# Kernel optimization log

Hardware: AMD Instinct MI355X
Metric: run time of the kernel (lower is better)

## Reference

```python
import jax, jax.numpy as jnp
import numpy as np

D_MODEL = 256
D_STATE = 64
D_CONV = 4
EXPAND = 2
HEADDIM = 16
D_INNER = EXPAND * D_MODEL            # 512
NHEADS = D_INNER // HEADDIM           # 32
CONV_DIM = D_INNER + 2 * D_STATE      # 640 (ngroups=1)
D_IN_PROJ = 2 * D_INNER + 2 * D_STATE + NHEADS  # 1184
BATCH = 256
SEQ = 200


def _ln(x, g, b, eps=1e-12):
    m = jnp.mean(x, axis=-1, keepdims=True)
    v = jnp.mean((x - m) ** 2, axis=-1, keepdims=True)
    return (x - m) * jax.lax.rsqrt(v + eps) * g + b


def setup_inputs() -> dict:
    key = jax.random.key(0)
    ks = jax.random.split(key, 16)
    def gn(i, shape, s=0.02):
        return jax.random.normal(ks[i], shape, jnp.float32) * s
    return {
        "input_tensor": jax.random.normal(ks[0], (BATCH, SEQ, D_MODEL), jnp.float32),
        # Mamba2 params
        "in_proj_w": gn(1, (D_MODEL, D_IN_PROJ)),
        "conv_w": gn(2, (CONV_DIM, D_CONV), 0.1),
        "conv_b": jnp.zeros((CONV_DIM,), jnp.float32),
        "dt_bias": gn(3, (NHEADS,), 0.1),
        "A_log": jnp.log(jax.random.uniform(ks[4], (NHEADS,), jnp.float32, 1.0, 16.0)),
        "D_skip": jnp.ones((NHEADS,), jnp.float32),
        "rms_w": jnp.ones((D_INNER,), jnp.float32),
        "out_proj_w": gn(5, (D_INNER, D_MODEL)),
        # Layer norms / mixers
        "ln_g": jnp.ones((D_MODEL,), jnp.float32),
        "ln_b": jnp.zeros((D_MODEL,), jnp.float32),
        "filt_w": gn(6, (1, SEQ // 2 + 1, D_MODEL, 2), 0.02),
        "filt_ln_g": jnp.ones((D_MODEL,), jnp.float32),
        "filt_ln_b": jnp.zeros((D_MODEL,), jnp.float32),
        "alpha": jax.random.uniform(ks[7], (D_MODEL,), jnp.float32),
        "beta": jax.random.uniform(ks[8], (D_MODEL,), jnp.float32),
        # FFN
        "ffn_w1": gn(9, (D_MODEL, 4 * D_MODEL)),
        "ffn_b1": jnp.zeros((4 * D_MODEL,), jnp.float32),
        "ffn_w2": gn(10, (4 * D_MODEL, D_MODEL)),
        "ffn_b2": jnp.zeros((D_MODEL,), jnp.float32),
        "ffn_ln_g": jnp.ones((D_MODEL,), jnp.float32),
        "ffn_ln_b": jnp.zeros((D_MODEL,), jnp.float32),
    }


def _mamba2(x, in_proj_w, conv_w, conv_b, dt_bias, A_log, D_skip, rms_w, out_proj_w):
    b, l, _ = x.shape
    zxbcdt = x @ in_proj_w                                  # [b,l,1184]
    z, xBC, dt = jnp.split(zxbcdt, [D_INNER, D_INNER + CONV_DIM], axis=-1)
    # depthwise causal conv over time + SiLU
    xp = jnp.pad(xBC, ((0, 0), (D_CONV - 1, 0), (0, 0)))
    conv = conv_b + sum(conv_w[:, k] * xp[:, k:k + l, :] for k in range(D_CONV))
    xBC = jax.nn.silu(conv)
    xs, Bm, Cm = jnp.split(xBC, [D_INNER, D_INNER + D_STATE], axis=-1)
    xh = xs.reshape(b, l, NHEADS, HEADDIM)
    dt = jax.nn.softplus(dt + dt_bias)                      # [b,l,h]
    A = -jnp.exp(A_log)                                     # [h]
    dA = jnp.exp(dt * A)                                    # [b,l,h]
    dtx = dt[..., None] * xh                                # [b,l,h,p]

    def step(state, inp):
        dA_t, dtx_t, B_t, C_t = inp
        # state: [b,h,p,n]
        state = dA_t[:, :, None, None] * state + dtx_t[..., None] * B_t[:, None, None, :]
        y_t = jnp.einsum('bhpn,bn->bhp', state, C_t)
        return state, y_t

    state0 = jnp.zeros((b, NHEADS, HEADDIM, D_STATE), x.dtype)
    _, y = jax.lax.scan(step, state0,
                        (jnp.moveaxis(dA, 1, 0), jnp.moveaxis(dtx, 1, 0),
                         jnp.moveaxis(Bm, 1, 0), jnp.moveaxis(Cm, 1, 0)))
    y = jnp.moveaxis(y, 0, 1) + D_skip[None, None, :, None] * xh   # skip connection
    y = y.reshape(b, l, D_INNER)
    # gated RMSNorm: rmsnorm(y * silu(z)) * w
    g = y * jax.nn.silu(z)
    g = g * jax.lax.rsqrt(jnp.mean(g * g, axis=-1, keepdims=True) + 1e-5) * rms_w
    return g @ out_proj_w


def reference(input_tensor, in_proj_w, conv_w, conv_b, dt_bias, A_log, D_skip,
              rms_w, out_proj_w, ln_g, ln_b, filt_w, filt_ln_g, filt_ln_b,
              alpha, beta, ffn_w1, ffn_b1, ffn_w2, ffn_b2, ffn_ln_g, ffn_ln_b):
    x = input_tensor
    h1 = _mamba2(x, in_proj_w, conv_w, conv_b, dt_bias, A_log, D_skip, rms_w, out_proj_w)
    h1 = _ln(h1 + x, ln_g, ln_b)
    # FFT filter branch
    xf = jnp.fft.rfft(x, axis=1, norm='ortho')
    w = filt_w[..., 0] + 1j * filt_w[..., 1]                # [1,101,d]
    xi = jnp.fft.irfft(xf * w, n=SEQ, axis=1, norm='ortho').astype(x.dtype)
    h2 = _ln(xi + x, filt_ln_g, filt_ln_b)
    h = alpha * h1 + beta * h2
    hid = jax.nn.gelu(h @ ffn_w1 + ffn_b1, approximate=False) @ ffn_w2 + ffn_b2
    return _ln(hid + h, ffn_ln_g, ffn_ln_b)
```

## Files before the change

### kernel.cpp

```cpp
#include <hip/hip_runtime.h>
#include <math.h>

#define BATCHN 256
#define SEQ 200
#define DMODEL 256
#define DINNER 512
#define NH 32
#define HD 16
#define DSTATE 64
#define DINPROJ 1184
#define XBCLD 672
#define BL (BATCHN*SEQ)
#define NF 101
#define XBASE 655360
#define TC 20
#define NCH 10
#define XIOFF 8500000

typedef __attribute__((ext_vector_type(8))) short bf16x8;
typedef __attribute__((ext_vector_type(4))) float f32x4;

__device__ inline unsigned short f2bf(float f) {
    union { float f; unsigned u; } v; v.f = f;
    unsigned r = v.u + 0x7FFFu + ((v.u >> 16) & 1u);
    return (unsigned short)(r >> 16);
}
__device__ inline float bf2f(unsigned short h) {
    union { unsigned u; float f; } v; v.u = ((unsigned)h) << 16;
    return v.f;
}

#define GLOAD16(src, dst) __builtin_amdgcn_global_load_lds( \
    (const __attribute__((address_space(1))) void*)(src),   \
    (__attribute__((address_space(3))) void*)(dst), 16, 0, 0)

__global__ void init_dft_kernel(unsigned short* __restrict__ EF, unsigned short* __restrict__ EI)
{
    const float ang = 6.28318530717958647692f / 200.0f;
    int idx = blockIdx.x * 256 + threadIdx.x;
    if (idx < 256 * SEQ) {
        int f = idx / SEQ, t = idx - f * SEQ;
        float v;
        if (f <= 100) { int ph = (f * t) % 200; v = cosf(ang * (float)ph); }
        else if (f <= 201) { int ff = f - 101; int ph = (ff * t) % 200; v = -sinf(ang * (float)ph); }
        else v = 0.f;
        EF[idx] = f2bf(v);
    } else if (idx < 256 * SEQ + 256 * 256) {
        int j2 = idx - 256 * SEQ;
        int t = j2 >> 8, j = j2 & 255;
        float v;
        if (t >= 200) v = 0.f;
        else if (j == 0) v = 1.0f / 200.0f;
        else if (j == 100) v = ((t & 1) ? -1.0f : 1.0f) / 200.0f;
        else if (j < 100) { int ph = (j * t) % 200; v = 2.0f * cosf(ang * (float)ph) / 200.0f; }
        else if (j >= 202 || j == 101 || j == 201) v = 0.0f;
        else { int f = j - 101; int ph = (f * t) % 200; v = -2.0f * sinf(ang * (float)ph) / 200.0f; }
        EI[j2] = f2bf(v);
    }
}

#define S0 303104
#define S1 131072
#define S2 262144
#define S3 262144
#define S4 1638400
__global__ void setup_kernel(const float* __restrict__ ipw, const float* __restrict__ opw,
                             const float* __restrict__ w1, const float* __restrict__ w2,
                             const float* __restrict__ X,
                             unsigned short* __restrict__ wTall, unsigned short* __restrict__ opwT,
                             unsigned short* __restrict__ w1T, unsigned short* __restrict__ w2T,
                             unsigned short* __restrict__ xbf)
{
    long long idx = (long long)blockIdx.x * 256 + threadIdx.x;
    if (idx < S0) { int n = (int)(idx / 256), k = (int)(idx % 256);
        wTall[idx] = f2bf(ipw[(long long)k * DINPROJ + n]); return; }
    idx -= S0;
    if (idx < S1) { int n = (int)(idx / 512), k = (int)(idx % 512);
        opwT[idx] = f2bf(opw[(long long)k * 256 + n]); return; }
    idx -= S1;
    if (idx < S2) { int n = (int)(idx / 256), k = (int)(idx % 256);
        w1T[idx] = f2bf(w1[(long long)k * 1024 + n]); return; }
    idx -= S2;
    if (idx < S3) { int n = (int)(idx / 1024), k = (int)(idx % 1024);
        w2T[idx] = f2bf(w2[(long long)k * 256 + n]); return; }
    idx -= S3;
    if (idx < S4) {
        long long i = idx * 8;
        float4 a = ((const float4*)(X + i))[0];
        float4 b = ((const float4*)(X + i))[1];
        uint4 o;
        o.x = (unsigned)f2bf(a.x) | ((unsigned)f2bf(a.y) << 16);
        o.y = (unsigned)f2bf(a.z) | ((unsigned)f2bf(a.w) << 16);
        o.z = (unsigned)f2bf(b.x) | ((unsigned)f2bf(b.y) << 16);
        o.w = (unsigned)f2bf(b.z) | ((unsigned)f2bf(b.w) << 16);
        *(uint4*)(xbf + i) = o;
    }
}

__global__ void xT_kernel(const float* __restrict__ X, unsigned short* __restrict__ XT)
{
    __shared__ float tile[32][33];
    int b = blockIdx.z, t0 = blockIdx.x * 32, d0 = blockIdx.y * 32;
    int tx = threadIdx.x & 31, ty = threadIdx.x >> 5;
    const float* xb = X + (long long)b * SEQ * DMODEL;
#pragma unroll
    for (int i = 0; i < 4; i++) {
        int t = t0 + ty + i * 8;
        tile[ty + i * 8][tx] = (t < SEQ) ? xb[(long long)t * DMODEL + d0 + tx] : 0.f;
    }
    __syncthreads();
    unsigned short* xtb = XT + (long long)b * DMODEL * SEQ;
#pragma unroll
    for (int i = 0; i < 4; i++) {
        int d = d0 + ty + i * 8;
        int t = t0 + tx;
        if (t < SEQ) xtb[(long long)d * SEQ + t] = f2bf(tile[tx][ty + i * 8]);
    }
}

template<int ACT, int CBF>
__global__ __launch_bounds__(256) void mgemm_kernel(
    const unsigned short* __restrict__ Ab, const unsigned short* __restrict__ BTp,
    void* __restrict__ Cp, const float* __restrict__ bias,
    int M, int N, int K, int lda, int ldbt, int ldc,
    long long sA, long long sBT, long long sC)
{
    __shared__ unsigned short As[128 * 32];
    __shared__ unsigned short Bs[128 * 32];
    const unsigned short* Aa = Ab + (long long)blockIdx.z * sA;
    const unsigned short* Bt = BTp + (long long)blockIdx.z * sBT;
    float* Cf = (float*)Cp + (CBF ? 0 : (long long)blockIdx.z * sC);
    unsigned short* Cb = (unsigned short*)Cp + (CBF ? (long long)blockIdx.z * sC : 0);

    int m0 = blockIdx.y * 128, n0 = blockIdx.x * 128;
    int tid = threadIdx.x;
    int srow = tid >> 1, skb = (tid & 1) * 16;
    int w = tid >> 6, l = tid & 63;
    int wr = w >> 1, wc = w & 1;
    int fr = l & 15, fk = l >> 4;
    int glr = (w << 4) + (l >> 2);
    int glc = (l & 3) << 3;
    bool fullM = (m0 + 128 <= M);
    bool fullN = (n0 + 128 <= N);

    f32x4 acc[4][4] = {};

    for (int k0 = 0; k0 < K; k0 += 32) {
        bool kedge = (k0 + 32 > K);
        if (fullM && !kedge) {
            GLOAD16(Aa + (long long)(m0 + glr) * lda + k0 + glc,      &As[w << 9]);
            GLOAD16(Aa + (long long)(m0 + 64 + glr) * lda + k0 + glc, &As[2048 + (w << 9)]);
        } else {
            int gm = m0 + srow;
            unsigned short* dst = &As[srow * 32 + skb];
#pragma unroll
            for (int i = 0; i < 16; i++) {
                int gk = k0 + skb + i;
                dst[i] = (gm < M && gk < K) ? Aa[(long long)gm * lda + gk] : (unsigned short)0;
            }
        }
        if (fullN && !kedge) {
            GLOAD16(Bt + (long long)(n0 + glr) * ldbt + k0 + glc,      &Bs[w << 9]);
            GLOAD16(Bt + (long long)(n0 + 64 + glr) * ldbt + k0 + glc, &Bs[2048 + (w << 9)]);
        } else {
            int gn = n0 + srow;
            unsigned short* dst = &Bs[srow * 32 + skb];
#pragma unroll
            for (int i = 0; i < 16; i++) {
                int gk = k0 + skb + i;
                dst[i] = (gn < N && gk < K) ? Bt[(long long)gn * ldbt + gk] : (unsigned short)0;
            }
        }
        __syncthreads();
        bf16x8 a[4], b[4];
#pragma unroll
        for (int i = 0; i < 4; i++) {
            a[i] = *(const bf16x8*)&As[(wr * 64 + i * 16 + fr) * 32 + fk * 8];
            b[i] = *(const bf16x8*)&Bs[(wc * 64 + i * 16 + fr) * 32 + fk * 8];
        }
#pragma unroll
        for (int i = 0; i < 4; i++)
#pragma unroll
            for (int j = 0; j < 4; j++)
                acc[i][j] = __builtin_amdgcn_mfma_f32_16x16x32_bf16(a[i], b[j], acc[i][j], 0, 0, 0);
        __syncthreads();
    }

#pragma unroll
    for (int i = 0; i < 4; i++) {
        int gr0 = m0 + wr * 64 + i * 16 + fk * 4;
#pragma unroll
        for (int j = 0; j < 4; j++) {
            int gc = n0 + wc * 64 + j * 16 + fr;
            if (gc >= N) continue;
            float bv = bias ? bias[gc] : 0.f;
#pragma unroll
            for (int r = 0; r < 4; r++) {
                int gr = gr0 + r;
                if (gr >= M) continue;
                float v = acc[i][j][r] + bv;
                if (ACT == 1) v = 0.5f * v * (1.f + erff(v * 0.70710678118654752f));
                long long ci = (long long)gr * ldc + gc;
                if (CBF) Cb[ci] = f2bf(v);
                else Cf[ci] = v;
            }
        }
    }
}

__global__ __launch_bounds__(256) void mgemm_proj(
    const unsigned short* __restrict__ Aa, const unsigned short* __restrict__ Bt,
    float* __restrict__ XBCout, unsigned short* __restrict__ Zout)
{
    __shared__ unsigned short As[128 * 32];
    __shared__ unsigned short Bs[128 * 32];
    const int N = DINPROJ;
    int m0 = blockIdx.y * 128, n0 = blockIdx.x * 128;
    int tid = threadIdx.x;
    int srow = tid >> 1, skb = (tid & 1) * 16;
    int w = tid >> 6, l = tid & 63;
    int wr = w >> 1, wc = w & 1;
    int fr = l & 15, fk = l >> 4;
    int glr = (w << 4) + (l >> 2);
    int glc = (l & 3) << 3;
    bool fullN = (n0 + 128 <= N);

    f32x4 acc[4][4] = {};

    for (int k0 = 0; k0 < 256; k0 += 32) {
        GLOAD16(Aa + (long long)(m0 + glr) * 256 + k0 + glc,      &As[w << 9]);
        GLOAD16(Aa + (long long)(m0 + 64 + glr) * 256 + k0 + glc, &As[2048 + (w << 9)]);
        if (fullN) {
            GLOAD16(Bt + (long long)(n0 + glr) * 256 + k0 + glc,      &Bs[w << 9]);
            GLOAD16(Bt + (long long)(n0 + 64 + glr) * 256 + k0 + glc, &Bs[2048 + (w << 9)]);
        } else {
            int gn = n0 + srow;
            unsigned short* dst = &Bs[srow * 32 + skb];
#pragma unroll
            for (int i = 0; i < 16; i++)
                dst[i] = (gn < N) ? Bt[(long long)gn * 256 + k0 + skb + i] : (unsigned short)0;
        }
        __syncthreads();
        bf16x8 a[4], b[4];
#pragma unroll
        for (int i = 0; i < 4; i++) {
            a[i] = *(const bf16x8*)&As[(wr * 64 + i * 16 + fr) * 32 + fk * 8];
            b[i] = *(const bf16x8*)&Bs[(wc * 64 + i * 16 + fr) * 32 + fk * 8];
        }
#pragma unroll
        for (int i = 0; i < 4; i++)
#pragma unroll
            for (int j = 0; j < 4; j++)
                acc[i][j] = __builtin_amdgcn_mfma_f32_16x16x32_bf16(a[i], b[j], acc[i][j], 0, 0, 0);
        __syncthreads();
    }

#pragma unroll
    for (int i = 0; i < 4; i++) {
        int gr0 = m0 + wr * 64 + i * 16 + fk * 4;
#pragma unroll
        for (int j = 0; j < 4; j++) {
            int gc = n0 + wc * 64 + j * 16 + fr;
            if (gc >= N) continue;
#pragma unroll
            for (int r = 0; r < 4; r++) {
                int gr = gr0 + r;
                float v = acc[i][j][r];
                if (gc < 512) Zout[(long long)gr * 512 + gc] = f2bf(v);
                else XBCout[(long long)gr * XBCLD + (gc - 512)] = v;
            }
        }
    }
}

__global__ __launch_bounds__(256) void convbc2_kernel(
    const float* __restrict__ XBC, const float* __restrict__ conv_w,
    const float* __restrict__ conv_b, const float* __restrict__ dt_bias,
    const float* __restrict__ A_log,
    float* __restrict__ BCb, float* __restrict__ DTb, float* __restrict__ DAb,
    float* __restrict__ BCF)
{
    __shared__ float swin[28][128];
    __shared__ float sv[25][128];
    int tid = threadIdx.x;
    int bid = blockIdx.x;
    int b = bid >> 3, c = bid & 7;
    int t0 = c * 25;
    long long rowb = (long long)b * SEQ;
    for (int i = tid; i < 28 * 32; i += 256) {
        int r = i >> 5, q = i & 31;
        int t = t0 - 3 + r;
        float4 v = (t >= 0) ? ((const float4*)(XBC + (rowb + t) * XBCLD + 512))[q]
                            : (float4){0.f, 0.f, 0.f, 0.f};
        ((float4*)&swin[r][0])[q] = v;
    }
    for (int i = tid; i < 25 * 32; i += 256) {
        int r = i >> 5, h = i & 31;
        long long row = rowb + t0 + r;
        float draw = XBC[row * XBCLD + 640 + h] + dt_bias[h];
        float dtv = (draw > 20.f) ? draw : log1pf(__expf(draw));
        DTb[row * NH + h] = dtv;
        DAb[row * NH + h] = __expf(-__expf(A_log[h]) * dtv);
    }
    __syncthreads();
    for (int i = tid; i < 25 * 128; i += 256) {
        int r = i >> 7, ch = i & 127;
        int gch = 512 + ch;
        float acc = conv_b[gch];
#pragma unroll
        for (int k = 0; k < 4; k++)
            acc = fmaf(conv_w[gch * 4 + k], swin[r + k][ch], acc);
        float v = acc * __builtin_amdgcn_rcpf(1.f + __expf(-acc));
        BCb[(rowb + t0 + r) * 128 + ch] = v;
        sv[r][ch] = v;
    }
    __syncthreads();
    int wv = tid >> 6, lane = tid & 63;
    for (int r = wv; r < 25; r += 4) {
        float prod = sv[r][lane] * sv[r][64 + lane];
#pragma unroll
        for (int m = 1; m < 64; m <<= 1) prod += __shfl_xor(prod, m);
        if (lane == 0) BCF[rowb + t0 + r] = prod;
    }
}

__device__ __forceinline__ void sstep2(
    float raw, float dtv, float da, float bc,
    const float4& qb0, const float4& qb1, const float4& qb2, const float4& qb3,
    const float4& qc0, const float4& qc1, const float4& qc2, const float4& qc3,
    float cw0, float cw1, float cw2, float cw3, float cb, float ds,
    float* st, float& w0, float& w1, float& w2,
    int lane, float* __restrict__ yaddr)
{
    float cvv = cb + cw0 * w0 + cw1 * w1 + cw2 * w2 + cw3 * raw;
    float xhv = cvv * __builtin_amdgcn_rcpf(1.f + __expf(-cvv));
    w0 = w1; w1 = w2; w2 = raw;
    float xv = dtv * xhv;
    float p0 = st[0]  * qc0.x;
    float p1 = st[1]  * qc0.y;
    float p2 = st[2]  * qc0.z;
    float p3 = st[3]  * qc0.w;
    p0 = fmaf(st[4],  qc1.x, p0);
    p1 = fmaf(st[5],  qc1.y, p1);
    p2 = fmaf(st[6],  qc1.z, p2);
    p3 = fmaf(st[7],  qc1.w, p3);
    p0 = fmaf(st[8],  qc2.x, p0);
    p1 = fmaf(st[9],  qc2.y, p1);
    p2 = fmaf(st[10], qc2.z, p2);
    p3 = fmaf(st[11], qc2.w, p3);
    p0 = fmaf(st[12], qc3.x, p0);
    p1 = fmaf(st[13], qc3.y, p1);
    p2 = fmaf(st[14], qc3.z, p2);
    p3 = fmaf(st[15], qc3.w, p3);
    st[0]  = fmaf(da, st[0],  xv * qb0.x);
    st[1]  = fmaf(da, st[1],  xv * qb0.y);
    st[2]  = fmaf(da, st[2],  xv * qb0.z);
    st[3]  = fmaf(da, st[3],  xv * qb0.w);
    st[4]  = fmaf(da, st[4],  xv * qb1.x);
    st[5]  = fmaf(da, st[5],  xv * qb1.y);
    st[6]  = fmaf(da, st[6],  xv * qb1.z);
    st[7]  = fmaf(da, st[7],  xv * qb1.w);
    st[8]  = fmaf(da, st[8],  xv * qb2.x);
    st[9]  = fmaf(da, st[9],  xv * qb2.y);
    st[10] = fmaf(da, st[10], xv * qb2.z);
    st[11] = fmaf(da, st[11], xv * qb2.w);
    st[12] = fmaf(da, st[12], xv * qb3.x);
    st[13] = fmaf(da, st[13], xv * qb3.y);
    st[14] = fmaf(da, st[14], xv * qb3.z);
    st[15] = fmaf(da, st[15], xv * qb3.w);
    float part = (p0 + p1) + (p2 + p3);
    part += __shfl_xor(part, 16);
    part += __shfl_xor(part, 32);
    if (lane < HD) *yaddr = fmaf(da, part, fmaf(xv, bc, ds * xhv));
}

__global__ __launch_bounds__(256) void scan7b_kernel(
    const float* __restrict__ DTb, const float* __restrict__ DAb,
    float* __restrict__ XBC, const float* __restrict__ BCb,
    const float* __restrict__ Dsk,
    const float* __restrict__ conv_w, const float* __restrict__ conv_b,
    const float* __restrict__ BCF)
{
    __shared__ float sbc[2][TC][128];
    __shared__ unsigned short sx[2][TC][128];
    __shared__ float sdt[2][TC][8];
    __shared__ float sda[2][TC][8];
    __shared__ float sbcf[2][TC];
    int tid = threadIdx.x;
    int wv = tid >> 6, lane = tid & 63;
    int bid = blockIdx.x;
    int b = bid >> 2, hq = (bid & 3) * 8;
    long long rowb = (long long)b * SEQ;

    for (int i = tid; i < TC * 32; i += 256) {
        int r = i >> 5, c = i & 31;
        ((float4*)&sbc[0][r][0])[c] = ((const float4*)(BCb + (rowb + r) * 128))[c];
    }
    for (int i = tid; i < TC * 64; i += 256) {
        int r = i >> 6, c2 = i & 63;
        float2 v = *(const float2*)(XBC + (rowb + r) * XBCLD + hq * 16 + (c2 << 1));
        *(unsigned*)&sx[0][r][c2 << 1] = (unsigned)f2bf(v.x) | ((unsigned)f2bf(v.y) << 16);
    }
    for (int i = tid; i < TC * 8; i += 256) {
        int t = i >> 3, j = i & 7;
        sdt[0][t][j] = DTb[(rowb + t) * NH + hq + j];
        sda[0][t][j] = DAb[(rowb + t) * NH + hq + j];
    }
    if (tid < TC) sbcf[0][tid] = BCF[rowb + tid];
    __syncthreads();

    int p = lane & 15, g = lane >> 4;
    int hA = hq + wv, hB = hq + 4 + wv;
    int chA = hA * HD + p, chB = hB * HD + p;
    float cwA0 = conv_w[chA * 4 + 0], cwA1 = conv_w[chA * 4 + 1];
    float cwA2 = conv_w[chA * 4 + 2], cwA3 = conv_w[chA * 4 + 3];
    float cbA = conv_b[chA];
    float cwB0 = conv_w[chB * 4 + 0], cwB1 = conv_w[chB * 4 + 1];
    float cwB2 = conv_w[chB * 4 + 2], cwB3 = conv_w[chB * 4 + 3];
    float cbB = conv_b[chB];
    float dsA = Dsk[hA], dsB = Dsk[hB];
    int xcA = wv * 16 + p, xcB = (4 + wv) * 16 + p;
    float* ypA = XBC + rowb * XBCLD + hA * HD + p;
    float* ypB = XBC + rowb * XBCLD + hB * HD + p;
    float stA[16], stB[16];
#pragma unroll
    for (int r = 0; r < 16; r++) { stA[r] = 0.f; stB[r] = 0.f; }
    float wA0 = 0.f, wA1 = 0.f, wA2 = 0.f;
    float wB0 = 0.f, wB1 = 0.f, wB2 = 0.f;

    for (int c = 0; c < NCH; c++) {
        int cur = c & 1;
        if (c + 1 < NCH) {
            int nb = cur ^ 1;
            long long tb = rowb + (c + 1) * TC;
            for (int i = tid; i < TC * 32; i += 256) {
                int r = i >> 5, cc = i & 31;
                ((float4*)&sbc[nb][r][0])[cc] = ((const float4*)(BCb + (tb + r) * 128))[cc];
            }
            for (int i = tid; i < TC * 64; i += 256) {
                int r = i >> 6, c2 = i & 63;
                float2 v = *(const float2*)(XBC + (tb + r) * XBCLD + hq * 16 + (c2 << 1));
                *(unsigned*)&sx[nb][r][c2 << 1] = (unsigned)f2bf(v.x) | ((unsigned)f2bf(v.y) << 16);
            }
            for (int i = tid; i < TC * 8; i += 256) {
                int t = i >> 3, j = i & 7;
                sdt[nb][t][j] = DTb[(tb + t) * NH + hq + j];
                sda[nb][t][j] = DAb[(tb + t) * NH + hq + j];
            }
            if (tid < TC) sbcf[nb][tid] = BCF[tb + tid];
        }
        int tbase = c * TC;
        for (int t = 0; t < TC; t++) {
            int gt = tbase + t;
            const float4* qb = (const float4*)&sbc[cur][t][g * 16];
            const float4* qc = (const float4*)&sbc[cur][t][64 + g * 16];
            float4 qb0 = qb[0], qb1 = qb[1], qb2 = qb[2], qb3 = qb[3];
            float4 qc0 = qc[0], qc1 = qc[1], qc2 = qc[2], qc3 = qc[3];
            float rawA = bf2f(sx[cur][t][xcA]);
            float rawB = bf2f(sx[cur][t][xcB]);
            float bc = sbcf[cur][t];
            sstep2(rawA, sdt[cur][t][wv], sda[cur][t][wv], bc,
                   qb0, qb1, qb2, qb3, qc0, qc1, qc2, qc3,
                   cwA0, cwA1, cwA2, cwA3, cbA, dsA, stA, wA0, wA1, wA2,
                   lane, ypA + (long long)gt * XBCLD);
            sstep2(rawB, sdt[cur][t][4 + wv], sda[cur][t][4 + wv], bc,
                   qb0, qb1, qb2, qb3, qc0, qc1, qc2, qc3,
                   cwB0, cwB1, cwB2, cwB3, cbB, dsB, stB, wB0, wB1, wB2,
                   lane, ypB + (long long)gt * XBCLD);
        }
        __syncthreads();
    }
}

__global__ __launch_bounds__(256) void gate_kernel(
    float* __restrict__ XBC, const unsigned short* __restrict__ Zbf,
    const float* __restrict__ rms_w)
{
    int row = blockIdx.x * 4 + (threadIdx.x >> 6);
    int lane = threadIdx.x & 63;
    float* yrow = XBC + (long long)row * XBCLD + lane * 8;
    const unsigned short* zrow = Zbf + (long long)row * 512 + lane * 8;
    float4 y0 = ((const float4*)yrow)[0];
    float4 y1 = ((const float4*)yrow)[1];
    uint4 zq = ((const uint4*)zrow)[0];
    float yv[8] = { y0.x, y0.y, y0.z, y0.w, y1.x, y1.y, y1.z, y1.w };
    float zv[8];
    zv[0] = bf2f((unsigned short)(zq.x & 0xFFFF)); zv[1] = bf2f((unsigned short)(zq.x >> 16));
    zv[2] = bf2f((unsigned short)(zq.y & 0xFFFF)); zv[3] = bf2f((unsigned short)(zq.y >> 16));
    zv[4] = bf2f((unsigned short)(zq.z & 0xFFFF)); zv[5] = bf2f((unsigned short)(zq.z >> 16));
    zv[6] = bf2f((unsigned short)(zq.w & 0xFFFF)); zv[7] = bf2f((unsigned short)(zq.w >> 16));
    float a[8]; float ss = 0.f;
#pragma unroll
    for (int i = 0; i < 8; i++) {
        float z = zv[i];
        a[i] = yv[i] * (z * __builtin_amdgcn_rcpf(1.f + __expf(-z)));
        ss = fmaf(a[i], a[i], ss);
    }
#pragma unroll
    for (int m = 1; m < 64; m <<= 1) ss += __shfl_xor(ss, m);
    float sc = rsqrtf(ss * (1.f / 512.f) + 1e-5f);
    const float* rw = rms_w + lane * 8;
    float4 r0 = ((const float4*)rw)[0];
    float4 r1 = ((const float4*)rw)[1];
    float rv[8] = { r0.x, r0.y, r0.z, r0.w, r1.x, r1.y, r1.z, r1.w };
    uint4 o;
    o.x = (unsigned)f2bf(a[0] * sc * rv[0]) | ((unsigned)f2bf(a[1] * sc * rv[1]) << 16);
    o.y = (unsigned)f2bf(a[2] * sc * rv[2]) | ((unsigned)f2bf(a[3] * sc * rv[3]) << 16);
    o.z = (unsigned)f2bf(a[4] * sc * rv[4]) | ((unsigned)f2bf(a[5] * sc * rv[5]) << 16);
    o.w = (unsigned)f2bf(a[6] * sc * rv[6]) | ((unsigned)f2bf(a[7] * sc * rv[7]) << 16);
    unsigned short* grow = (unsigned short*)(XBC + (long long)row * XBCLD);
    ((uint4*)grow)[lane] = o;
}

__global__ void lnadd_bb_kernel(const unsigned short* __restrict__ A, const unsigned short* __restrict__ Bb,
                                const float* __restrict__ g, const float* __restrict__ be,
                                float* __restrict__ O)
{
    int row = blockIdx.x * 4 + (threadIdx.x >> 6);
    int lane = threadIdx.x & 63;
    long long base = (long long)row * DMODEL + lane * 4;
    float v[4]; float s1 = 0.f;
#pragma unroll
    for (int i = 0; i < 4; i++) { float a = bf2f(A[base + i]) + bf2f(Bb[base + i]); v[i] = a; s1 += a; }
#pragma unroll
    for (int m = 1; m < 64; m <<= 1) s1 += __shfl_xor(s1, m);
    float mean = s1 * (1.f / 256.f);
    float s2 = 0.f;
#pragma unroll
    for (int i = 0; i < 4; i++) { float d = v[i] - mean; s2 = fmaf(d, d, s2); }
#pragma unroll
    for (int m = 1; m < 64; m <<= 1) s2 += __shfl_xor(s2, m);
    float r = rsqrtf(s2 * (1.f / 256.f) + 1e-12f);
#pragma unroll
    for (int i = 0; i < 4; i++)
        O[base + i] = (v[i] - mean) * r * g[lane * 4 + i] + be[lane * 4 + i];
}

__global__ void combine2_kernel(const float* __restrict__ XI, const float* __restrict__ X,
                                const float* __restrict__ MO, unsigned short* __restrict__ HB,
                                const float* __restrict__ lg, const float* __restrict__ lb,
                                const float* __restrict__ fg, const float* __restrict__ fb,
                                const float* __restrict__ al, const float* __restrict__ bt)
{
    int row = blockIdx.x * 4 + (threadIdx.x >> 6);
    int lane = threadIdx.x & 63;
    long long base = (long long)row * DMODEL + lane * 4;
    int bb = row / SEQ, ll = row - bb * SEQ;
    long long xib = (long long)bb * 65536 + ll * 256 + lane * 4;
    float u[4], v[4]; float su = 0.f, sv = 0.f;
#pragma unroll
    for (int i = 0; i < 4; i++) {
        float xv = X[base + i];
        float a = MO[base + i] + xv;
        float b = XI[xib + i] + xv;
        u[i] = a; v[i] = b; su += a; sv += b;
    }
#pragma unroll
    for (int m = 1; m < 64; m <<= 1) { su += __shfl_xor(su, m); sv += __shfl_xor(sv, m); }
    float mu = su * (1.f / 256.f), mv = sv * (1.f / 256.f);
    float qu = 0.f, qv = 0.f;
#pragma unroll
    for (int i = 0; i < 4; i++) {
        float du = u[i] - mu; qu = fmaf(du, du, qu);
        float dv = v[i] - mv; qv = fmaf(dv, dv, qv);
    }
#pragma unroll
    for (int m = 1; m < 64; m <<= 1) { qu += __shfl_xor(qu, m); qv += __shfl_xor(qv, m); }
    float ru = rsqrtf(qu * (1.f / 256.f) + 1e-12f);
    float rv = rsqrtf(qv * (1.f / 256.f) + 1e-12f);
#pragma unroll
    for (int i = 0; i < 4; i++) {
        int d = lane * 4 + i;
        float h1 = (u[i] - mu) * ru * lg[d] + lb[d];
        float h2 = (v[i] - mv) * rv * fg[d] + fb[d];
        float h = al[d] * h1 + bt[d] * h2;
        HB[base + i] = f2bf(h);
    }
}

__global__ void filt_kernel(unsigned short* __restrict__ XF, const float* __restrict__ W)
{
    long long idx = (long long)blockIdx.x * 256 + threadIdx.x;
    if (idx >= (long long)BATCHN * DMODEL * NF) return;
    int f = (int)(idx % NF);
    int d = (int)((idx / NF) % DMODEL);
    int b = (int)(idx / ((long long)NF * DMODEL));
    long long base = ((long long)b * DMODEL + d) * 256;
    float re = bf2f(XF[base + f]);
    float im = bf2f(XF[base + 101 + f]);
    float wr = W[((long long)f * DMODEL + d) * 2];
    float wi = W[((long long)f * DMODEL + d) * 2 + 1];
    XF[base + f]       = f2bf(re * wr - im * wi);
    XF[base + 101 + f] = f2bf(re * wi + im * wr);
}

extern "C" void kernel_launch(void* const* d_in, const int* in_sizes, int n_in,
                              void* d_out, int out_size, void* d_ws, size_t ws_size,
                              hipStream_t stream)
{
    const float* x          = (const float*)d_in[0];
    const float* in_proj_w  = (const float*)d_in[1];
    const float* conv_w     = (const float*)d_in[2];
    const float* conv_b     = (const float*)d_in[3];
    const float* dt_bias    = (const float*)d_in[4];
    const float* A_log      = (const float*)d_in[5];
    const float* D_skip     = (const float*)d_in[6];
    const float* rms_w      = (const float*)d_in[7];
    const float* out_proj_w = (const float*)d_in[8];
    const float* ln_g       = (const float*)d_in[9];
    const float* ln_b       = (const float*)d_in[10];
    const float* filt_w     = (const float*)d_in[11];
    const float* filt_ln_g  = (const float*)d_in[12];
    const float* filt_ln_b  = (const float*)d_in[13];
    const float* alpha      = (const float*)d_in[14];
    const float* beta       = (const float*)d_in[15];
    const float* ffn_w1     = (const float*)d_in[16];
    const float* ffn_b1     = (const float*)d_in[17];
    const float* ffn_w2     = (const float*)d_in[18];
    const float* ffn_b2     = (const float*)d_in[19];
    const float* ffn_ln_g   = (const float*)d_in[20];
    const float* ffn_ln_b   = (const float*)d_in[21];
    float* out = (float*)d_out;
    float* ws = (float*)d_ws;

    unsigned short* WP    = (unsigned short*)(ws + 81920);
    unsigned short* wTall = WP;
    unsigned short* opwT  = wTall + 1184 * 256;
    unsigned short* w1T   = opwT + 256 * 512;
    unsigned short* w2T   = w1T + 1024 * 256;
    unsigned short* EFbf  = w2T + 256 * 1024;
    unsigned short* EIbf  = EFbf + 256 * SEQ;
    float* XBC = ws + XBASE;
    float* BCb = XBC + (long long)BL * XBCLD;
    float* DTb = BCb + (long long)BL * 128;
    float* DAb = DTb + (long long)BL * NH;
    float* MO  = DAb + (long long)BL * NH;
    float* BCF = MO + (long long)BL * DMODEL;
    unsigned short* Zbf = (unsigned short*)MO;
    unsigned short* xbf  = (unsigned short*)BCb;
    unsigned short* xTbf = (unsigned short*)BCb;
    unsigned short* MObf = (unsigned short*)BCb;
    unsigned short* Gbf = (unsigned short*)XBC;
    unsigned short* XFT = (unsigned short*)XBC;
    float* XI  = XBC + XIOFF;
    unsigned short* HID = (unsigned short*)XBC;
    unsigned short* FFO = (unsigned short*)(XBC + 26500000);

    init_dft_kernel<<<dim3((256 * SEQ + 256 * 256 + 255) / 256), dim3(256), 0, stream>>>(EFbf, EIbf);
    setup_kernel<<<dim3((S0 + S1 + S2 + S3 + S4) / 256), dim3(256), 0, stream>>>(
        in_proj_w, out_proj_w, ffn_w1, ffn_w2, x, wTall, opwT, w1T, w2T, xbf);

    mgemm_proj<<<dim3(10, BL / 128), dim3(256), 0, stream>>>(xbf, wTall, XBC, Zbf);

    convbc2_kernel<<<dim3(BATCHN * 8), dim3(256), 0, stream>>>(XBC, conv_w, conv_b, dt_bias,
                                                               A_log, BCb, DTb, DAb, BCF);

    scan7b_kernel<<<dim3(BATCHN * 4), dim3(256), 0, stream>>>(DTb, DAb, XBC, BCb, D_skip,
                                                              conv_w, conv_b, BCF);

    xT_kernel<<<dim3(7, 8, BATCHN), dim3(256), 0, stream>>>(x, xTbf);

    gate_kernel<<<dim3(BL / 4), dim3(256), 0, stream>>>(XBC, Zbf, rms_w);

    mgemm_kernel<0,0><<<dim3(2, BL / 128, 1), dim3(256), 0, stream>>>(
        Gbf, opwT, MO, nullptr, BL, 256, 512, 1344, 512, 256, 0, 0, 0);

    mgemm_kernel<0,1><<<dim3(2, 2, BATCHN), dim3(256), 0, stream>>>(
        xTbf, EFbf, XFT, nullptr, 256, 256, SEQ, SEQ, SEQ, 256,
        (long long)DMODEL * SEQ, 0, 65536);

    filt_kernel<<<dim3((BATCHN * DMODEL * NF + 255) / 256), dim3(256), 0, stream>>>(XFT, filt_w);

    mgemm_kernel<0,0><<<dim3(2, 2, BATCHN), dim3(256), 0, stream>>>(
        EIbf, XFT, XI, nullptr, 256, 256, 256, 256, 256, 256,
        0, 65536, 65536);

    combine2_kernel<<<dim3(BL / 4), dim3(256), 0, stream>>>(XI, x, MO, MObf,
                                                            ln_g, ln_b, filt_ln_g, filt_ln_b,
                                                            alpha, beta);

    mgemm_kernel<1,1><<<dim3(8, BL / 128, 1), dim3(256), 0, stream>>>(
        MObf, w1T, HID, ffn_b1, BL, 1024, 256, 256, 256, 1024, 0, 0, 0);

    mgemm_kernel<0,1><<<dim3(2, BL / 128, 1), dim3(256), 0, stream>>>(
        HID, w2T, FFO, ffn_b2, BL, 256, 1024, 1024, 1024, 256, 0, 0, 0);

    lnadd_bb_kernel<<<dim3(BL / 4), dim3(256), 0, stream>>>(FFO, MObf, ffn_ln_g, ffn_ln_b, out);
}
```

Before: 790.5 us.

## Double GEMM K-tile to 64 and store inverse-DFT output as bf16

```diff
diff --git a/kernel.cpp b/kernel.cpp
--- a/kernel.cpp
+++ b/kernel.cpp
@@ -125,8 +125,8 @@
     int M, int N, int K, int lda, int ldbt, int ldc,
     long long sA, long long sBT, long long sC)
 {
-    __shared__ unsigned short As[128 * 32];
-    __shared__ unsigned short Bs[128 * 32];
+    __shared__ unsigned short As[128 * 64];
+    __shared__ unsigned short Bs[128 * 64];
     const unsigned short* Aa = Ab + (long long)blockIdx.z * sA;
     const unsigned short* Bt = BTp + (long long)blockIdx.z * sBT;
     float* Cf = (float*)Cp + (CBF ? 0 : (long long)blockIdx.z * sC);
@@ -134,55 +134,62 @@
 
     int m0 = blockIdx.y * 128, n0 = blockIdx.x * 128;
     int tid = threadIdx.x;
-    int srow = tid >> 1, skb = (tid & 1) * 16;
     int w = tid >> 6, l = tid & 63;
     int wr = w >> 1, wc = w & 1;
     int fr = l & 15, fk = l >> 4;
-    int glr = (w << 4) + (l >> 2);
-    int glc = (l & 3) << 3;
+    int grow = (w & 1) * 64 + (l >> 2);
+    int gcol = (w >> 1) * 32 + (l & 3) * 8;
+    int srow = tid >> 1, shalf = tid & 1;
     bool fullM = (m0 + 128 <= M);
     bool fullN = (n0 + 128 <= N);
 
     f32x4 acc[4][4] = {};
 
-    for (int k0 = 0; k0 < K; k0 += 32) {
-        bool kedge = (k0 + 32 > K);
+    for (int k0 = 0; k0 < K; k0 += 64) {
+        bool kedge = (k0 + 64 > K);
         if (fullM && !kedge) {
-            GLOAD16(Aa + (long long)(m0 + glr) * lda + k0 + glc,      &As[w << 9]);
-            GLOAD16(Aa + (long long)(m0 + 64 + glr) * lda + k0 + glc, &As[2048 + (w << 9)]);
+#pragma unroll
+            for (int q = 0; q < 4; q++)
+                GLOAD16(Aa + (long long)(m0 + grow + q * 16) * lda + k0 + gcol,
+                        &As[w * 2048 + q * 512]);
         } else {
             int gm = m0 + srow;
-            unsigned short* dst = &As[srow * 32 + skb];
-#pragma unroll
-            for (int i = 0; i < 16; i++) {
-                int gk = k0 + skb + i;
+            unsigned short* dst = &As[shalf * 4096 + srow * 32];
+#pragma unroll
+            for (int i = 0; i < 32; i++) {
+                int gk = k0 + shalf * 32 + i;
                 dst[i] = (gm < M && gk < K) ? Aa[(long long)gm * lda + gk] : (unsigned short)0;
             }
         }
         if (fullN && !kedge) {
-            GLOAD16(Bt + (long long)(n0 + glr) * ldbt + k0 + glc,      &Bs[w << 9]);
-            GLOAD16(Bt + (long long)(n0 + 64 + glr) * ldbt + k0 + glc, &Bs[2048 + (w << 9)]);
+#pragma unroll
+            for (int q = 0; q < 4; q++)
+                GLOAD16(Bt + (long long)(n0 + grow + q * 16) * ldbt + k0 + gcol,
+                        &Bs[w * 2048 + q * 512]);
         } else {
             int gn = n0 + srow;
-            unsigned short* dst = &Bs[srow * 32 + skb];
-#pragma unroll
-            for (int i = 0; i < 16; i++) {
-                int gk = k0 + skb + i;
+            unsigned short* dst = &Bs[shalf * 4096 + srow * 32];
+#pragma unroll
+            for (int i = 0; i < 32; i++) {
+                int gk = k0 + shalf * 32 + i;
                 dst[i] = (gn < N && gk < K) ? Bt[(long long)gn * ldbt + gk] : (unsigned short)0;
             }
         }
         __syncthreads();
-        bf16x8 a[4], b[4];
-#pragma unroll
-        for (int i = 0; i < 4; i++) {
-            a[i] = *(const bf16x8*)&As[(wr * 64 + i * 16 + fr) * 32 + fk * 8];
-            b[i] = *(const bf16x8*)&Bs[(wc * 64 + i * 16 + fr) * 32 + fk * 8];
-        }
-#pragma unroll
-        for (int i = 0; i < 4; i++)
-#pragma unroll
-            for (int j = 0; j < 4; j++)
-                acc[i][j] = __builtin_amdgcn_mfma_f32_16x16x32_bf16(a[i], b[j], acc[i][j], 0, 0, 0);
+#pragma unroll
+        for (int s = 0; s < 2; s++) {
+            bf16x8 a[4], b[4];
+#pragma unroll
+            for (int i = 0; i < 4; i++) {
+                a[i] = *(const bf16x8*)&As[s * 4096 + (wr * 64 + i * 16 + fr) * 32 + fk * 8];
+                b[i] = *(const bf16x8*)&Bs[s * 4096 + (wc * 64 + i * 16 + fr) * 32 + fk * 8];
+            }
+#pragma unroll
+            for (int i = 0; i < 4; i++)
+#pragma unroll
+                for (int j = 0; j < 4; j++)
+                    acc[i][j] = __builtin_amdgcn_mfma_f32_16x16x32_bf16(a[i], b[j], acc[i][j], 0, 0, 0);
+        }
         __syncthreads();
     }
 
@@ -212,46 +219,55 @@
     const unsigned short* __restrict__ Aa, const unsigned short* __restrict__ Bt,
     float* __restrict__ XBCout, unsigned short* __restrict__ Zout)
 {
-    __shared__ unsigned short As[128 * 32];
-    __shared__ unsigned short Bs[128 * 32];
+    __shared__ unsigned short As[128 * 64];
+    __shared__ unsigned short Bs[128 * 64];
     const int N = DINPROJ;
     int m0 = blockIdx.y * 128, n0 = blockIdx.x * 128;
     int tid = threadIdx.x;
-    int srow = tid >> 1, skb = (tid & 1) * 16;
     int w = tid >> 6, l = tid & 63;
     int wr = w >> 1, wc = w & 1;
     int fr = l & 15, fk = l >> 4;
-    int glr = (w << 4) + (l >> 2);
-    int glc = (l & 3) << 3;
+    int grow = (w & 1) * 64 + (l >> 2);
+    int gcol = (w >> 1) * 32 + (l & 3) * 8;
+    int srow = tid >> 1, shalf = tid & 1;
     bool fullN = (n0 + 128 <= N);
 
     f32x4 acc[4][4] = {};
 
-    for (int k0 = 0; k0 < 256; k0 += 32) {
-        GLOAD16(Aa + (long long)(m0 + glr) * 256 + k0 + glc,      &As[w << 9]);
-        GLOAD16(Aa + (long long)(m0 + 64 + glr) * 256 + k0 + glc, &As[2048 + (w << 9)]);
+    for (int k0 = 0; k0 < 256; k0 += 64) {
+#pragma unroll
+        for (int q = 0; q < 4; q++)
+            GLOAD16(Aa + (long long)(m0 + grow + q * 16) * 256 + k0 + gcol,
+                    &As[w * 2048 + q * 512]);
         if (fullN) {
-            GLOAD16(Bt + (long long)(n0 + glr) * 256 + k0 + glc,      &Bs[w << 9]);
-            GLOAD16(Bt + (long long)(n0 + 64 + glr) * 256 + k0 + glc, &Bs[2048 + (w << 9)]);
+#pragma unroll
+            for (int q = 0; q < 4; q++)
+                GLOAD16(Bt + (long long)(n0 + grow + q * 16) * 256 + k0 + gcol,
+                        &Bs[w * 2048 + q * 512]);
         } else {
             int gn = n0 + srow;
-            unsigned short* dst = &Bs[srow * 32 + skb];
-#pragma unroll
-            for (int i = 0; i < 16; i++)
-                dst[i] = (gn < N) ? Bt[(long long)gn * 256 + k0 + skb + i] : (unsigned short)0;
+            unsigned short* dst = &Bs[shalf * 4096 + srow * 32];
+#pragma unroll
+            for (int i = 0; i < 32; i++) {
+                int gk = k0 + shalf * 32 + i;
+                dst[i] = (gn < N) ? Bt[(long long)gn * 256 + gk] : (unsigned short)0;
+            }
         }
         __syncthreads();
-        bf16x8 a[4], b[4];
-#pragma unroll
-        for (int i = 0; i < 4; i++) {
-            a[i] = *(const bf16x8*)&As[(wr * 64 + i * 16 + fr) * 32 + fk * 8];
-            b[i] = *(const bf16x8*)&Bs[(wc * 64 + i * 16 + fr) * 32 + fk * 8];
-        }
-#pragma unroll
-        for (int i = 0; i < 4; i++)
-#pragma unroll
-            for (int j = 0; j < 4; j++)
-                acc[i][j] = __builtin_amdgcn_mfma_f32_16x16x32_bf16(a[i], b[j], acc[i][j], 0, 0, 0);
+#pragma unroll
+        for (int s = 0; s < 2; s++) {
+            bf16x8 a[4], b[4];
+#pragma unroll
+            for (int i = 0; i < 4; i++) {
+                a[i] = *(const bf16x8*)&As[s * 4096 + (wr * 64 + i * 16 + fr) * 32 + fk * 8];
+                b[i] = *(const bf16x8*)&Bs[s * 4096 + (wc * 64 + i * 16 + fr) * 32 + fk * 8];
+            }
+#pragma unroll
+            for (int i = 0; i < 4; i++)
+#pragma unroll
+                for (int j = 0; j < 4; j++)
+                    acc[i][j] = __builtin_amdgcn_mfma_f32_16x16x32_bf16(a[i], b[j], acc[i][j], 0, 0, 0);
+        }
         __syncthreads();
     }
 
@@ -536,7 +552,7 @@
         O[base + i] = (v[i] - mean) * r * g[lane * 4 + i] + be[lane * 4 + i];
 }
 
-__global__ void combine2_kernel(const float* __restrict__ XI, const float* __restrict__ X,
+__global__ void combine2_kernel(const unsigned short* __restrict__ XI, const float* __restrict__ X,
                                 const float* __restrict__ MO, unsigned short* __restrict__ HB,
                                 const float* __restrict__ lg, const float* __restrict__ lb,
                                 const float* __restrict__ fg, const float* __restrict__ fb,
@@ -552,7 +568,7 @@
     for (int i = 0; i < 4; i++) {
         float xv = X[base + i];
         float a = MO[base + i] + xv;
-        float b = XI[xib + i] + xv;
+        float b = bf2f(XI[xib + i]) + xv;
         u[i] = a; v[i] = b; su += a; sv += b;
     }
 #pragma unroll
@@ -642,7 +658,7 @@
     unsigned short* MObf = (unsigned short*)BCb;
     unsigned short* Gbf = (unsigned short*)XBC;
     unsigned short* XFT = (unsigned short*)XBC;
-    float* XI  = XBC + XIOFF;
+    unsigned short* XI  = (unsigned short*)(XBC + XIOFF);
     unsigned short* HID = (unsigned short*)XBC;
     unsigned short* FFO = (unsigned short*)(XBC + 26500000);
 
@@ -671,7 +687,7 @@
 
     filt_kernel<<<dim3((BATCHN * DMODEL * NF + 255) / 256), dim3(256), 0, stream>>>(XFT, filt_w);
 
-    mgemm_kernel<0,0><<<dim3(2, 2, BATCHN), dim3(256), 0, stream>>>(
+    mgemm_kernel<0,1><<<dim3(2, 2, BATCHN), dim3(256), 0, stream>>>(
         EIbf, XFT, XI, nullptr, 256, 256, 256, 256, 256, 256,
         0, 65536, 65536);
 
```

After: 804.5 us. No clear change (+1.8%).
